# Optimization experiments

Measured on AMD Instinct MI355X. Metric: run time of the kernel, lower is better.

The kernel has to match this reference:

```python
import jax, jax.numpy as jnp
import numpy as np

B, L, D0, H, K = 16, 256, 64, 128, 512  # batch, seq, feat, hidden, codebook size


def _p(key, shape, scale=0.05):
    return jax.random.normal(key, shape, jnp.float32) * scale


def setup_inputs() -> dict:
    key = jax.random.key(0)
    ks = jax.random.split(key, 32)
    inp = {
        "inputs": jax.random.normal(ks[0], (B, L, D0), jnp.float32),
        "input_lens": jnp.full((B,), L, dtype=jnp.int64),
        "in_mask": jnp.ones((B, L), jnp.float32),
        # encoder params
        "enc_lin1_W": _p(ks[1], (H, D0)), "enc_lin1_b": jnp.zeros((H,), jnp.float32),
        "enc_Wih_f": _p(ks[2], (4 * H, H)), "enc_Whh_f": _p(ks[3], (4 * H, H)), "enc_b_f": jnp.zeros((4 * H,), jnp.float32),
        "enc_Wih_b": _p(ks[4], (4 * H, H)), "enc_Whh_b": _p(ks[5], (4 * H, H)), "enc_b_b": jnp.zeros((4 * H,), jnp.float32),
        "enc_lin2_W": _p(ks[6], (H, 2 * H)), "enc_lin2_b": jnp.zeros((H,), jnp.float32),
        # VQ codebook (K codes of dim H), init uniform(-1/K, 1/K) as in torch
        "vq_emb": jax.random.uniform(ks[7], (K, H), jnp.float32, -1.0 / K, 1.0 / K),
        # decoder params
        "dec_lin1_W": _p(ks[8], (H, D0)), "dec_lin1_b": jnp.zeros((H,), jnp.float32),
        "dec_Wih": _p(ks[9], (4 * H, H)), "dec_Whh": _p(ks[10], (4 * H, H)), "dec_b": jnp.zeros((4 * H,), jnp.float32),
        "attn_Wq": _p(ks[11], (H, H)), "attn_bq": jnp.zeros((H,), jnp.float32),
        "attn_Wk": _p(ks[12], (H, H)), "attn_bk": jnp.zeros((H,), jnp.float32),
        "attn_Wv": _p(ks[13], (H, H)), "attn_bv": jnp.zeros((H,), jnp.float32),
        "dec_lin2_W": _p(ks[14], (D0, H)), "dec_lin2_b": jnp.zeros((D0,), jnp.float32),
    }
    return inp


def _lstm_cell(x, h, c, Wih, Whh, b):
    g = x @ Wih.T + h @ Whh.T + b  # (B, 4H)
    i, f, gg, o = jnp.split(g, 4, axis=-1)
    c = jax.nn.sigmoid(f) * c + jax.nn.sigmoid(i) * jnp.tanh(gg)
    h = jax.nn.sigmoid(o) * jnp.tanh(c)
    return h, c


def _lstm_scan(x_blh, Wih, Whh, b, reverse=False):
    Bb = x_blh.shape[0]
    Hh = Whh.shape[1]
    init = (jnp.zeros((Bb, Hh), x_blh.dtype), jnp.zeros((Bb, Hh), x_blh.dtype))

    def step(carry, x):
        h, c = _lstm_cell(x, carry[0], carry[1], Wih, Whh, b)
        return (h, c), h

    _, hs = jax.lax.scan(step, init, jnp.swapaxes(x_blh, 0, 1), reverse=reverse)
    return jnp.swapaxes(hs, 0, 1)  # (B, L, H)


def _forward(inputs, in_mask, p):
    # ---- encoder: Linear -> ReLU -> BiLSTM -> Linear (full-length sequences) ----
    enc_x = jax.nn.relu(inputs @ p["enc_lin1_W"].T + p["enc_lin1_b"])
    hf = _lstm_scan(enc_x, p["enc_Wih_f"], p["enc_Whh_f"], p["enc_b_f"], reverse=False)
    hb = _lstm_scan(enc_x, p["enc_Wih_b"], p["enc_Whh_b"], p["enc_b_b"], reverse=True)
    ze = jnp.concatenate([hf, hb], axis=-1) @ p["enc_lin2_W"].T + p["enc_lin2_b"]  # (B,L,H)

    # ---- VQ: nearest codebook entry (expanded ||a-b||^2, avoids (B,L,K,C) tensor) ----
    emb = p["vq_emb"]  # (K, H)
    dist = (jnp.sum(ze * ze, -1, keepdims=True)
            - 2.0 * jnp.einsum("blc,kc->blk", ze, emb)
            + jnp.sum(emb * emb, -1)[None, None, :])  # (B,L,K)
    nearest = jnp.argmin(dist, axis=-1)  # (B,L) int
    zq = emb[nearest]  # (B,L,H)
    dec_in = ze + jax.lax.stop_gradient(zq - ze)  # straight-through

    k_proj = dec_in @ p["attn_Wk"].T + p["attn_bk"]  # (B,L,H)
    v_proj = dec_in @ p["attn_Wv"].T + p["attn_bv"]
    scale = 1.0 / jnp.sqrt(jnp.float32(H))
    mask_add = jnp.where(in_mask == 0, -1e9, 0.0).astype(jnp.float32)  # (B,L)

    def dec_step(carry, _):
        h, c, tok = carry
        x = jax.nn.relu(tok @ p["dec_lin1_W"].T + p["dec_lin1_b"])  # (B,H)
        h, c = _lstm_cell(x, h, c, p["dec_Wih"], p["dec_Whh"], p["dec_b"])
        q = h @ p["attn_Wq"].T + p["attn_bq"]  # (B,H)
        scores = jnp.einsum("bd,bld->bl", q, k_proj) * scale + mask_add
        attn = jax.nn.softmax(scores, axis=-1)  # (B,L)
        ctx = jnp.einsum("bl,bld->bd", attn, v_proj)  # (B,H)
        out = ctx @ p["dec_lin2_W"].T + p["dec_lin2_b"]  # (B,D0)
        return (h, c, out), (out, attn)

    Bb = inputs.shape[0]
    init = (jnp.zeros((Bb, H), jnp.float32), jnp.zeros((Bb, H), jnp.float32), jnp.zeros((Bb, D0), jnp.float32))
    _, (outs, attns) = jax.lax.scan(dec_step, init, None, length=dec_in.shape[1])
    dec_out = jnp.swapaxes(outs, 0, 1)  # (B,L,D0)
    attn_w = jnp.swapaxes(attns, 0, 1)  # (B,L,L)
    return dec_out, attn_w, ze, zq


def reference(inputs, input_lens, in_mask, enc_lin1_W, enc_lin1_b, enc_Wih_f, enc_Whh_f, enc_b_f,
              enc_Wih_b, enc_Whh_b, enc_b_b, enc_lin2_W, enc_lin2_b, vq_emb,
              dec_lin1_W, dec_lin1_b, dec_Wih, dec_Whh, dec_b,
              attn_Wq, attn_bq, attn_Wk, attn_bk, attn_Wv, attn_bv, dec_lin2_W, dec_lin2_b):
    p = dict(enc_lin1_W=enc_lin1_W, enc_lin1_b=enc_lin1_b, enc_Wih_f=enc_Wih_f, enc_Whh_f=enc_Whh_f,
             enc_b_f=enc_b_f, enc_Wih_b=enc_Wih_b, enc_Whh_b=enc_Whh_b, enc_b_b=enc_b_b,
             enc_lin2_W=enc_lin2_W, enc_lin2_b=enc_lin2_b, vq_emb=vq_emb,
             dec_lin1_W=dec_lin1_W, dec_lin1_b=dec_lin1_b, dec_Wih=dec_Wih, dec_Whh=dec_Whh, dec_b=dec_b,
             attn_Wq=attn_Wq, attn_bq=attn_bq, attn_Wk=attn_Wk, attn_bk=attn_bk,
             attn_Wv=attn_Wv, attn_bv=attn_bv, dec_lin2_W=dec_lin2_W, dec_lin2_b=dec_lin2_b)
    return _forward(inputs, in_mask, p)
```

## Files before the change

### kernel.cpp

```cpp
#include <hip/hip_runtime.h>

#define Bn  16
#define Ln  256
#define D0n 64
#define Hn  128
#define H4n 512
#define Kn  512
#define BLn 4096

typedef float f4 __attribute__((ext_vector_type(4)));
typedef unsigned long long u64;

__device__ __forceinline__ float sigf(float x) { return 1.0f / (1.0f + expf(-x)); }

__device__ __forceinline__ float fma4v(f4 w, f4 x, float acc) {
    acc = fmaf(w.x, x.x, acc);
    acc = fmaf(w.y, x.y, acc);
    acc = fmaf(w.z, x.z, acc);
    acc = fmaf(w.w, x.w, acc);
    return acc;
}

__device__ __forceinline__ float dotn(const f4* __restrict__ a,
                                      const f4* __restrict__ w, int n4) {
    float a0 = 0.f, a1 = 0.f, a2 = 0.f, a3 = 0.f;
    for (int i = 0; i < n4; i += 4) {
        a0 = fma4v(a[i], w[i], a0);
        a1 = fma4v(a[i + 1], w[i + 1], a1);
        a2 = fma4v(a[i + 2], w[i + 2], a2);
        a3 = fma4v(a[i + 3], w[i + 3], a3);
    }
    return (a0 + a1) + (a2 + a3);
}

__device__ __forceinline__ void tag_store(u64* p, float v, unsigned tag) {
    u64 pk = ((u64)tag << 32) | (u64)__float_as_uint(v);
    __hip_atomic_store(p, pk, __ATOMIC_RELAXED, __HIP_MEMORY_SCOPE_AGENT);
}
__device__ __forceinline__ float tag_poll(u64* p, unsigned tag) {
    u64 v;
    do {
        v = __hip_atomic_load(p, __ATOMIC_RELAXED, __HIP_MEMORY_SCOPE_AGENT);
    } while ((unsigned)(v >> 32) != tag);
    return __uint_as_float((unsigned)v);
}

__global__ __launch_bounds__(256)
void k_gemm(const float* __restrict__ X, const float* __restrict__ W,
            const float* __restrict__ b, float* __restrict__ Y,
            int K, int out_dim, int do_relu, float scale) {
    __shared__ f4 wt[4160];
    const int K4 = K >> 2;
    const int st = K4 + 1;
    const int lg = __ffs(K4) - 1;
    const int tid = threadIdx.x;
    const int c = tid & 63, rpart = tid >> 6;
    const f4* W4 = (const f4*)W;
    const int per = (64 * K4) >> 8;
    for (int i = 0; i < per; ++i) {
        int idx = i * 256 + tid;
        int row = idx >> lg, col = idx & (K4 - 1);
        wt[row * st + col] = W4[(size_t)(blockIdx.x * 64 + row) * K4 + col];
    }
    __syncthreads();
    const f4* X4 = (const f4*)X;
    const float bc = b ? b[blockIdx.x * 64 + c] : 0.f;
    const f4* wrow = wt + c * st;
    for (int i = 0; i < 16; ++i) {
        int r = blockIdx.y * 64 + i * 4 + rpart;
        const f4* xr = X4 + (size_t)r * K4;
        float a0 = 0.f, a1 = 0.f, a2 = 0.f, a3 = 0.f;
        for (int k = 0; k < K4; k += 4) {
            a0 = fma4v(wrow[k],     xr[k],     a0);
            a1 = fma4v(wrow[k + 1], xr[k + 1], a1);
            a2 = fma4v(wrow[k + 2], xr[k + 2], a2);
            a3 = fma4v(wrow[k + 3], xr[k + 3], a3);
        }
        float acc = scale * ((a0 + a1) + (a2 + a3)) + bc;
        if (do_relu) acc = fmaxf(acc, 0.f);
        Y[(size_t)r * out_dim + blockIdx.x * 64 + c] = acc;
    }
}

__global__ void k_prep(const float* __restrict__ attn_Wq, float* __restrict__ WqT,
                       const f4* __restrict__ dec_Wih, f4* __restrict__ WihL,
                       const f4* __restrict__ whf, const f4* __restrict__ whb,
                       f4* __restrict__ WhhL, int* __restrict__ zbuf) {
    const int blk = blockIdx.x, tid = threadIdx.x;
    if (blk < 64) {
        int idx = blk * 256 + tid;
        int c = idx >> 7, r = idx & 127;
        WqT[idx] = attn_Wq[(size_t)r * Hn + c];
    } else if (blk < 128) {
        int idx = (blk - 64) * 256 + tid;
        int t = idx & 511, side = (idx >> 9) & 1, k = idx >> 10;
        int rl = t >> 1;
        int grow = (rl >> 6) * 128 + side * 64 + (rl & 63);
        WihL[idx] = dec_Wih[(size_t)grow * 32 + (t & 1) * 16 + k];
    } else if (blk < 192) {
        int idx = (blk - 128) * 256 + tid;
        int row = idx & 511, k = (idx >> 9) & 15, dir = idx >> 13;
        const f4* src = dir ? whb : whf;
        WhhL[idx] = src[(size_t)row * 32 + 16 + k];
    } else {
        int idx = (blk - 192) * 256 + tid;
        if (idx < 8192) zbuf[idx] = 0;
    }
}

__global__ void k_rearrKQF(const f4* __restrict__ in, f4* __restrict__ out) {
    int idx = blockIdx.x * blockDim.x + threadIdx.x;
    if (idx >= 131072) return;
    int tid = idx & 511, k = (idx >> 9) & 15, b = idx >> 13;
    out[idx] = in[((size_t)b * 256 + (tid >> 1)) * 32 + (tid & 1) * 16 + k];
}

__global__ void k_cst(const float* __restrict__ kp, const float* __restrict__ bq,
                      const float* __restrict__ mask, float* __restrict__ cst) {
    int p = blockIdx.x * blockDim.x + threadIdx.x;
    if (p >= BLn) return;
    float a = dotn((const f4*)bq, (const f4*)(kp + (size_t)p * Hn), Hn >> 2);
    cst[p] = a * 0.088388347648318447f + (mask[p] == 0.f ? -1e9f : 0.f);
}

__global__ void k_codenorm(const float* __restrict__ emb, float* __restrict__ c2) {
    int k = blockIdx.x * blockDim.x + threadIdx.x;
    if (k >= Kn) return;
    const f4* e4 = (const f4*)(emb + (size_t)k * Hn);
    float acc = 0.f;
    for (int i = 0; i < Hn / 4; ++i) {
        f4 v = e4[i];
        acc = fmaf(v.x, v.x, acc); acc = fmaf(v.y, v.y, acc);
        acc = fmaf(v.z, v.z, acc); acc = fmaf(v.w, v.w, acc);
    }
    c2[k] = acc;
}

__global__ __launch_bounds__(128)
void k_vqpick(const float* __restrict__ dist, const float* __restrict__ emb,
              float* __restrict__ zq) {
    const int p = blockIdx.x, tid = threadIdx.x;
    __shared__ int best_s;
    if (tid < 64) {
        float best = 3.0e38f; int bi = 0;
        for (int j = 0; j < 8; ++j) {
            int k = j * 64 + tid;
            float d = dist[(size_t)p * Kn + k];
            if (d < best) { best = d; bi = k; }
        }
        for (int off = 32; off > 0; off >>= 1) {
            float ov = __shfl_xor(best, off);
            int   oi = __shfl_xor(bi, off);
            if (ov < best || (ov == best && oi < bi)) { best = ov; bi = oi; }
        }
        if (tid == 0) best_s = bi;
    }
    __syncthreads();
    zq[(size_t)p * Hn + tid] = emb[(size_t)best_s * Hn + tid];
}

__global__ __launch_bounds__(512, 1)
void k_lstm3(const float* __restrict__ xWf, const float* __restrict__ xWb,
             const float* __restrict__ Whh_f, const float* __restrict__ Whh_b,
             const float* __restrict__ WhhL_g, float* __restrict__ hcat) {
    const int b   = blockIdx.x & 15;
    const int dir = blockIdx.x >> 4;
    const int tid = threadIdx.x;
    const float* xW  = dir ? xWb : xWf;
    const f4* Whh4   = (const f4*)(dir ? Whh_b : Whh_f);

    __shared__ __align__(16) f4 wh2_s[16 * 512];
    __shared__ __align__(16) float h_s[Hn];
    __shared__ float g_s[H4n];

    f4 w[16];
#pragma unroll
    for (int f = 0; f < 16; ++f) w[f] = Whh4[(size_t)tid * 32 + f];
#pragma unroll
    for (int f = 0; f < 16; ++f) asm volatile("" : "+v"(w[f]));

    const f4* WhhL4 = (const f4*)WhhL_g;
#pragma unroll
    for (int k = 0; k < 16; ++k)
        wh2_s[k * 512 + tid] = WhhL4[(size_t)dir * 8192 + k * 512 + tid];

    float c_reg = 0.f;
    if (tid < Hn) h_s[tid] = 0.f;

    const int t0 = dir ? (Ln - 1) : 0;
    float xw_v = xW[((size_t)b * Ln + t0) * H4n + tid];
    __syncthreads();

    for (int s = 0; s < Ln; ++s) {
        const int t = dir ? (Ln - 1 - s) : s;
        float xw_n = 0.f;
        if (s + 1 < Ln) {
            int tn = dir ? (Ln - 2 - s) : (s + 1);
            xw_n = xW[((size_t)b * Ln + tn) * H4n + tid];
        }
        {
            const f4* h4 = (const f4*)h_s;
            float a0 = 0.f, a1 = 0.f, a2 = 0.f, a3 = 0.f;
#pragma unroll
            for (int f = 0; f < 16; f += 4) {
                a0 = fma4v(w[f],     h4[f],     a0);
                a1 = fma4v(w[f + 1], h4[f + 1], a1);
                a2 = fma4v(w[f + 2], h4[f + 2], a2);
                a3 = fma4v(w[f + 3], h4[f + 3], a3);
            }
#pragma unroll
            for (int f = 0; f < 16; f += 4) {
                a0 = fma4v(wh2_s[f * 512 + tid],       h4[16 + f],     a0);
                a1 = fma4v(wh2_s[(f + 1) * 512 + tid], h4[16 + f + 1], a1);
                a2 = fma4v(wh2_s[(f + 2) * 512 + tid], h4[16 + f + 2], a2);
                a3 = fma4v(wh2_s[(f + 3) * 512 + tid], h4[16 + f + 3], a3);
            }
            g_s[tid] = (a0 + a1) + (a2 + a3) + xw_v;
        }
        __syncthreads();
        if (tid < Hn) {
            float ig = sigf(g_s[tid]);
            float fg = sigf(g_s[Hn + tid]);
            float gg = tanhf(g_s[2 * Hn + tid]);
            float og = sigf(g_s[3 * Hn + tid]);
            c_reg = fg * c_reg + ig * gg;
            float hv = og * tanhf(c_reg);
            h_s[tid] = hv;
            hcat[((size_t)b * Ln + t) * (2 * Hn) + dir * Hn + tid] = hv;
        }
        __syncthreads();
        xw_v = xw_n;
    }
}

__global__ __launch_bounds__(512, 1)
void k_decoder(const float* __restrict__ kqF_g, const float* __restrict__ vw_g,
               const float* __restrict__ cst_g,
               const float* __restrict__ W1,  const float* __restrict__ b1_g,
               const float* __restrict__ WihL_g, const float* __restrict__ Whh,
               const float* __restrict__ bd_g, u64* gxd,
               float* __restrict__ dec_out, float* __restrict__ attn_w) {
    const int b    = blockIdx.x & 15;
    const int side = blockIdx.x >> 4;
    const int tid  = threadIdx.x;

    __shared__ __align__(16) f4 wih_s[16 * 512];
    __shared__ __align__(16) float tok_s[D0n];
    __shared__ __align__(16) float x_s[Hn];
    __shared__ __align__(16) float h_s[Hn];
    __shared__ float g_loc[256];
    __shared__ float s_s[Ln];
    __shared__ float attn8[8][8][33];
    __shared__ float cst_s[Ln];
    __shared__ float b1_s[Hn];

    const int rl = tid >> 1, ghalf = tid & 1;
    const int grow = (rl >> 6) * 128 + side * 64 + (rl & 63);

    const f4* Whh4 = (const f4*)Whh;
    f4 whh[16];
#pragma unroll
    for (int f = 0; f < 16; ++f) whh[f] = Whh4[(size_t)grow * 32 + ghalf * 16 + f];
    float bdr = bd_g[grow];
    const int o = tid >> 3, slab = tid & 7;
    float vwr[32];
#pragma unroll
    for (int l = 0; l < 32; ++l)
        vwr[l] = vw_g[((size_t)b * Ln + slab * 32 + l) * D0n + o];
#pragma unroll
    for (int f = 0; f < 16; ++f) asm volatile("" : "+v"(whh[f]));
#pragma unroll
    for (int l = 0; l < 32; ++l) asm volatile("" : "+v"(vwr[l]));
    asm volatile("" : "+v"(bdr));

    const f4* WihL4 = (const f4*)WihL_g;
#pragma unroll
    for (int k = 0; k < 16; ++k)
        wih_s[k * 512 + tid] = WihL4[(size_t)k * 1024 + side * 512 + tid];
    if (tid < D0n) tok_s[tid] = 0.f;
    if (tid < Hn)  { h_s[tid] = 0.f; b1_s[tid] = b1_g[tid]; }
    if (tid < Ln)  cst_s[tid] = cst_g[(size_t)b * Ln + tid];
    float c_reg = 0.f;
    __syncthreads();

    u64* gx_mine = gxd + (b * 2 + side) * 128;
    u64* gx_peer = gxd + (b * 2 + (side ^ 1)) * 128;

    const int ar = tid >> 2, ap = tid & 3;
    const f4* W1_4 = (const f4*)W1;
    const f4* kqF  = (const f4*)kqF_g + (size_t)b * 8192;
    const int dbase = (tid & 1) * 16;
    const int wv = tid >> 6, lane = tid & 63;

    for (int t = 0; t < Ln; ++t) {
        {
            const f4* t4 = (const f4*)tok_s;
            float u0 = 0.f, u1 = 0.f;
#pragma unroll
            for (int k = 0; k < 4; k += 2) {
                f4 wa  = W1_4[(size_t)ar * 16 + ap * 4 + k];
                f4 wb2 = W1_4[(size_t)ar * 16 + ap * 4 + k + 1];
                u0 = fma4v(wa,  t4[ap * 4 + k],     u0);
                u1 = fma4v(wb2, t4[ap * 4 + k + 1], u1);
            }
            float a = u0 + u1;
            a += __shfl_xor(a, 1);
            a += __shfl_xor(a, 2);
            if (ap == 0) x_s[ar] = fmaxf(a + b1_s[ar], 0.f);
        }
        __syncthreads();
        {
            const f4* x4 = (const f4*)x_s + ghalf * 16;
            const f4* h4 = (const f4*)h_s + ghalf * 16;
            float a0 = 0.f, a1 = 0.f, a2 = 0.f, a3 = 0.f;
#pragma unroll
            for (int f = 0; f < 16; f += 4) {
                a0 = fma4v(wih_s[f * 512 + tid],       x4[f],     a0);
                a1 = fma4v(wih_s[(f + 1) * 512 + tid], x4[f + 1], a1);
                a2 = fma4v(wih_s[(f + 2) * 512 + tid], x4[f + 2], a2);
                a3 = fma4v(wih_s[(f + 3) * 512 + tid], x4[f + 3], a3);
            }
#pragma unroll
            for (int f = 0; f < 16; f += 4) {
                a0 = fma4v(whh[f],     h4[f],     a0);
                a1 = fma4v(whh[f + 1], h4[f + 1], a1);
                a2 = fma4v(whh[f + 2], h4[f + 2], a2);
                a3 = fma4v(whh[f + 3], h4[f + 3], a3);
            }
            float a = (a0 + a1) + (a2 + a3);
            a += __shfl_xor(a, 1);
            if (ghalf == 0) g_loc[rl] = a + bdr;
        }
        __syncthreads();
        if (tid < 64) {
            float ig = sigf(g_loc[tid]);
            float fg = sigf(g_loc[64 + tid]);
            float gg = tanhf(g_loc[128 + tid]);
            float og = sigf(g_loc[192 + tid]);
            c_reg = fg * c_reg + ig * gg;
            float hv = og * tanhf(c_reg);
            h_s[side * 64 + tid] = hv;
            tag_store(&gx_mine[(t & 1) * 64 + tid], hv, (unsigned)(t + 1));
            h_s[(side ^ 1) * 64 + tid] =
                tag_poll(&gx_peer[(t & 1) * 64 + tid], (unsigned)(t + 1));
        }
        __syncthreads();
        {
            const f4* h4 = (const f4*)h_s;
            float a0 = 0.f, a1 = 0.f;
#pragma unroll
            for (int k = 0; k < 16; k += 2) {
                f4 q0 = kqF[(size_t)k * 512 + tid];
                f4 q1 = kqF[(size_t)(k + 1) * 512 + tid];
                a0 = fma4v(q0, h4[dbase + k],     a0);
                a1 = fma4v(q1, h4[dbase + k + 1], a1);
            }
            float a = a0 + a1;
            a += __shfl_xor(a, 1);
            if ((tid & 1) == 0) s_s[tid >> 1] = a + cst_s[tid >> 1];
        }
        __syncthreads();
        {
            float v0 = s_s[lane],       v1 = s_s[lane + 64];
            float v2 = s_s[lane + 128], v3 = s_s[lane + 192];
            float m = fmaxf(fmaxf(v0, v1), fmaxf(v2, v3));
#pragma unroll
            for (int o2 = 32; o2 > 0; o2 >>= 1) m = fmaxf(m, __shfl_xor(m, o2));
            float e0 = expf(v0 - m), e1 = expf(v1 - m);
            float e2 = expf(v2 - m), e3 = expf(v3 - m);
            float ss = (e0 + e1) + (e2 + e3);
#pragma unroll
            for (int o2 = 32; o2 > 0; o2 >>= 1) ss += __shfl_xor(ss, o2);
            float inv = 1.f / ss;
            e0 *= inv; e1 *= inv; e2 *= inv; e3 *= inv;
            attn8[wv][lane >> 5][lane & 31] = e0;
            attn8[wv][(lane + 64) >> 5][lane & 31] = e1;
            attn8[wv][(lane + 128) >> 5][lane & 31] = e2;
            attn8[wv][(lane + 192) >> 5][lane & 31] = e3;
            if (side == 0 && wv == 0) {
                float* aw = attn_w + ((size_t)b * Ln + t) * Ln;
                aw[lane] = e0; aw[lane + 64] = e1;
                aw[lane + 128] = e2; aw[lane + 192] = e3;
            }
            asm volatile("s_waitcnt lgkmcnt(0)" ::: "memory");
            const float* as = attn8[wv][slab];
            float g0 = 0.f, g1 = 0.f, g2 = 0.f, g3 = 0.f;
#pragma unroll
            for (int l = 0; l < 32; l += 4) {
                g0 = fmaf(as[l],     vwr[l],     g0);
                g1 = fmaf(as[l + 1], vwr[l + 1], g1);
                g2 = fmaf(as[l + 2], vwr[l + 2], g2);
                g3 = fmaf(as[l + 3], vwr[l + 3], g3);
            }
            float a = (g0 + g1) + (g2 + g3);
            a += __shfl_xor(a, 1);
            a += __shfl_xor(a, 2);
            a += __shfl_xor(a, 4);
            if (slab == 0) {
                tok_s[o] = a;
                if (side == 1) dec_out[((size_t)b * Ln + t) * D0n + o] = a;
            }
        }
        __syncthreads();
    }
}

extern "C" void kernel_launch(void* const* d_in, const int* in_sizes, int n_in,
                              void* d_out, int out_size, void* d_ws, size_t ws_size,
                              hipStream_t stream) {
    const float* inputs     = (const float*)d_in[0];
    const float* in_mask    = (const float*)d_in[2];
    const float* enc_lin1_W = (const float*)d_in[3];
    const float* enc_lin1_b = (const float*)d_in[4];
    const float* enc_Wih_f  = (const float*)d_in[5];
    const float* enc_Whh_f  = (const float*)d_in[6];
    const float* enc_b_f    = (const float*)d_in[7];
    const float* enc_Wih_b  = (const float*)d_in[8];
    const float* enc_Whh_b  = (const float*)d_in[9];
    const float* enc_b_b    = (const float*)d_in[10];
    const float* enc_lin2_W = (const float*)d_in[11];
    const float* enc_lin2_b = (const float*)d_in[12];
    const float* vq_emb     = (const float*)d_in[13];
    const float* dec_lin1_W = (const float*)d_in[14];
    const float* dec_lin1_b = (const float*)d_in[15];
    const float* dec_Wih    = (const float*)d_in[16];
    const float* dec_Whh    = (const float*)d_in[17];
    const float* dec_b      = (const float*)d_in[18];
    const float* attn_Wq    = (const float*)d_in[19];
    const float* attn_bq    = (const float*)d_in[20];
    const float* attn_Wk    = (const float*)d_in[21];
    const float* attn_bk    = (const float*)d_in[22];
    const float* attn_Wv    = (const float*)d_in[23];
    const float* attn_bv    = (const float*)d_in[24];
    const float* dec_lin2_W = (const float*)d_in[25];
    const float* dec_lin2_b = (const float*)d_in[26];

    float* out     = (float*)d_out;
    float* dec_out = out;
    float* attn_w  = out + 262144;
    float* ze      = out + 1310720;
    float* zq      = out + 1835008;

    float* ws    = (float*)d_ws;
    float* enc_x = ws;
    float* xWf   = enc_x + 524288;
    float* xWb   = xWf + 2097152;
    float* hcat  = xWb + 2097152;
    float* kp    = hcat + 1048576;
    float* vp    = kp + 524288;
    float* c2    = vp + 524288;
    u64*   gxd   = (u64*)(c2 + 512);
    float* WqT   = enc_x;
    float* WihL  = enc_x + 16384;
    float* WhhL  = enc_x + 16384 + 65536;
    float* dist  = xWf;
    float* KQF   = xWf;
    float* kq    = xWb;
    float* vw    = xWb + 524288;
    float* cst   = xWb + 786432;

    dim3 blk(256);
    k_gemm<<<dim3(2, 64), blk, 0, stream>>>(inputs, enc_lin1_W, enc_lin1_b, enc_x, D0n, Hn, 1, 1.f);
    k_gemm<<<dim3(8, 64), blk, 0, stream>>>(enc_x, enc_Wih_f, enc_b_f, xWf, Hn, H4n, 0, 1.f);
    k_gemm<<<dim3(8, 64), blk, 0, stream>>>(enc_x, enc_Wih_b, enc_b_b, xWb, Hn, H4n, 0, 1.f);
    k_prep<<<224, 256, 0, stream>>>(attn_Wq, WqT, (const f4*)dec_Wih, (f4*)WihL,
                                    (const f4*)enc_Whh_f, (const f4*)enc_Whh_b,
                                    (f4*)WhhL, (int*)gxd);
    k_lstm3<<<32, 512, 0, stream>>>(xWf, xWb, enc_Whh_f, enc_Whh_b, WhhL, hcat);
    k_gemm<<<dim3(2, 64), blk, 0, stream>>>(hcat, enc_lin2_W, enc_lin2_b, ze, 2 * Hn, Hn, 0, 1.f);
    k_codenorm<<<2, 256, 0, stream>>>(vq_emb, c2);
    k_gemm<<<dim3(8, 64), blk, 0, stream>>>(ze, vq_emb, c2, dist, Hn, Kn, 0, -2.f);
    k_vqpick<<<BLn, 128, 0, stream>>>(dist, vq_emb, zq);
    k_gemm<<<dim3(2, 64), blk, 0, stream>>>(zq, attn_Wk, attn_bk, kp, Hn, Hn, 0, 1.f);
    k_gemm<<<dim3(2, 64), blk, 0, stream>>>(zq, attn_Wv, attn_bv, vp, Hn, Hn, 0, 1.f);
    k_gemm<<<dim3(2, 64), blk, 0, stream>>>(kp, WqT, nullptr, kq, Hn, Hn, 0, 0.088388347648318447f);
    k_rearrKQF<<<512, 256, 0, stream>>>((const f4*)kq, (f4*)KQF);
    k_gemm<<<dim3(1, 64), blk, 0, stream>>>(vp, dec_lin2_W, dec_lin2_b, vw, Hn, D0n, 0, 1.f);
    k_cst<<<Bn, 256, 0, stream>>>(kp, attn_bq, in_mask, cst);
    k_decoder<<<32, 512, 0, stream>>>(KQF, vw, cst,
                                      dec_lin1_W, dec_lin1_b,
                                      WihL, dec_Whh, dec_b, gxd,
                                      dec_out, attn_w);
}
```

Baseline: 1.633 ms.

## Transpose GEMM weight tile in LDS and compute decoder softmax once per block

The GEMM kernel now stores its weight tile transposed as scalars, column-major by k, so lanes read consecutive LDS words and X is loaded as f4 per thread. The old padded f4 row layout is gone. The decoder softmax, previously computed redundantly by all 8 wavefronts, is now done by the first wavefront only into a shared buffer, with an extra block barrier before the attention-weighted sum. This cuts redundant exp/shuffle work but adds a barrier to the serial timestep loop and leaves the other wavefronts idle during the softmax.

After: 1.644 ms. No clear change (+0.6%).

```diff
diff --git a/kernel.cpp b/kernel.cpp
--- a/kernel.cpp
+++ b/kernel.cpp
@@ -49,32 +49,33 @@
 void k_gemm(const float* __restrict__ X, const float* __restrict__ W,
             const float* __restrict__ b, float* __restrict__ Y,
             int K, int out_dim, int do_relu, float scale) {
-    __shared__ f4 wt[4160];
+    __shared__ float wtT[16384];
     const int K4 = K >> 2;
-    const int st = K4 + 1;
-    const int lg = __ffs(K4) - 1;
     const int tid = threadIdx.x;
     const int c = tid & 63, rpart = tid >> 6;
     const f4* W4 = (const f4*)W;
-    const int per = (64 * K4) >> 8;
-    for (int i = 0; i < per; ++i) {
-        int idx = i * 256 + tid;
-        int row = idx >> lg, col = idx & (K4 - 1);
-        wt[row * st + col] = W4[(size_t)(blockIdx.x * 64 + row) * K4 + col];
+    const int per = K4 >> 2;
+    for (int j = 0; j < per; ++j) {
+        int col = rpart * per + j;
+        f4 v = W4[(size_t)(blockIdx.x * 64 + c) * K4 + col];
+        wtT[(col * 4 + 0) * 64 + c] = v.x;
+        wtT[(col * 4 + 1) * 64 + c] = v.y;
+        wtT[(col * 4 + 2) * 64 + c] = v.z;
+        wtT[(col * 4 + 3) * 64 + c] = v.w;
     }
     __syncthreads();
     const f4* X4 = (const f4*)X;
     const float bc = b ? b[blockIdx.x * 64 + c] : 0.f;
-    const f4* wrow = wt + c * st;
     for (int i = 0; i < 16; ++i) {
         int r = blockIdx.y * 64 + i * 4 + rpart;
         const f4* xr = X4 + (size_t)r * K4;
         float a0 = 0.f, a1 = 0.f, a2 = 0.f, a3 = 0.f;
-        for (int k = 0; k < K4; k += 4) {
-            a0 = fma4v(wrow[k],     xr[k],     a0);
-            a1 = fma4v(wrow[k + 1], xr[k + 1], a1);
-            a2 = fma4v(wrow[k + 2], xr[k + 2], a2);
-            a3 = fma4v(wrow[k + 3], xr[k + 3], a3);
+        for (int k4 = 0; k4 < K4; ++k4) {
+            f4 xv = xr[k4];
+            a0 = fmaf(xv.x, wtT[(k4 * 4 + 0) * 64 + c], a0);
+            a1 = fmaf(xv.y, wtT[(k4 * 4 + 1) * 64 + c], a1);
+            a2 = fmaf(xv.z, wtT[(k4 * 4 + 2) * 64 + c], a2);
+            a3 = fmaf(xv.w, wtT[(k4 * 4 + 3) * 64 + c], a3);
         }
         float acc = scale * ((a0 + a1) + (a2 + a3)) + bc;
         if (do_relu) acc = fmaxf(acc, 0.f);
@@ -250,7 +251,7 @@
     __shared__ __align__(16) float h_s[Hn];
     __shared__ float g_loc[256];
     __shared__ float s_s[Ln];
-    __shared__ float attn8[8][8][33];
+    __shared__ float attn_sp[8][33];
     __shared__ float cst_s[Ln];
     __shared__ float b1_s[Hn];
 
@@ -290,7 +291,6 @@
     const f4* W1_4 = (const f4*)W1;
     const f4* kqF  = (const f4*)kqF_g + (size_t)b * 8192;
     const int dbase = (tid & 1) * 16;
-    const int wv = tid >> 6, lane = tid & 63;
 
     for (int t = 0; t < Ln; ++t) {
         {
@@ -360,9 +360,9 @@
             if ((tid & 1) == 0) s_s[tid >> 1] = a + cst_s[tid >> 1];
         }
         __syncthreads();
-        {
-            float v0 = s_s[lane],       v1 = s_s[lane + 64];
-            float v2 = s_s[lane + 128], v3 = s_s[lane + 192];
+        if (tid < 64) {
+            float v0 = s_s[tid],       v1 = s_s[tid + 64];
+            float v2 = s_s[tid + 128], v3 = s_s[tid + 192];
             float m = fmaxf(fmaxf(v0, v1), fmaxf(v2, v3));
 #pragma unroll
             for (int o2 = 32; o2 > 0; o2 >>= 1) m = fmaxf(m, __shfl_xor(m, o2));
@@ -373,17 +373,19 @@
             for (int o2 = 32; o2 > 0; o2 >>= 1) ss += __shfl_xor(ss, o2);
             float inv = 1.f / ss;
             e0 *= inv; e1 *= inv; e2 *= inv; e3 *= inv;
-            attn8[wv][lane >> 5][lane & 31] = e0;
-            attn8[wv][(lane + 64) >> 5][lane & 31] = e1;
-            attn8[wv][(lane + 128) >> 5][lane & 31] = e2;
-            attn8[wv][(lane + 192) >> 5][lane & 31] = e3;
-            if (side == 0 && wv == 0) {
+            attn_sp[tid >> 5][tid & 31] = e0;
+            attn_sp[(tid + 64) >> 5][tid & 31] = e1;
+            attn_sp[(tid + 128) >> 5][tid & 31] = e2;
+            attn_sp[(tid + 192) >> 5][tid & 31] = e3;
+            if (side == 0) {
                 float* aw = attn_w + ((size_t)b * Ln + t) * Ln;
-                aw[lane] = e0; aw[lane + 64] = e1;
-                aw[lane + 128] = e2; aw[lane + 192] = e3;
-            }
-            asm volatile("s_waitcnt lgkmcnt(0)" ::: "memory");
-            const float* as = attn8[wv][slab];
+                aw[tid] = e0; aw[tid + 64] = e1;
+                aw[tid + 128] = e2; aw[tid + 192] = e3;
+            }
+        }
+        __syncthreads();
+        {
+            const float* as = attn_sp[slab];
             float g0 = 0.f, g1 = 0.f, g2 = 0.f, g3 = 0.f;
 #pragma unroll
             for (int l = 0; l < 32; l += 4) {
```
